# Optimization experiments

Hardware: AMD Instinct MI355X
Metric: run time of the kernel (lower is better)

The kernel has to match this reference:

```python
import jax, jax.numpy as jnp
import numpy as np

HIDDEN = 1024
NUM_HEADS = 4
HEAD_DIM = HIDDEN // NUM_HEADS
SCALE = HEAD_DIM ** -0.5
EPS = 1e-5


def setup_inputs() -> dict:
    key = jax.random.key(0)
    ks = jax.random.split(key, 8)
    B, S, D = 4, 2048, HIDDEN
    x = jax.random.normal(ks[0], (B, S, D), dtype=jnp.float32)
    attention_mask = jnp.ones((B, S), dtype=jnp.int32)
    init = 1.0 / np.sqrt(D)
    Wq = jax.random.uniform(ks[1], (D, D), jnp.float32, -init, init)
    Wk = jax.random.uniform(ks[2], (D, D), jnp.float32, -init, init)
    Wv = jax.random.uniform(ks[3], (D, D), jnp.float32, -init, init)
    Wo = jax.random.uniform(ks[4], (D, D), jnp.float32, -init, init)
    bo = jax.random.uniform(ks[5], (D,), jnp.float32, -init, init)
    gamma = jnp.ones((D,), dtype=jnp.float32)
    beta = jnp.zeros((D,), dtype=jnp.float32)
    return {"x": x, "attention_mask": attention_mask, "Wq": Wq, "Wk": Wk,
            "Wv": Wv, "Wo": Wo, "bo": bo, "gamma": gamma, "beta": beta}


def reference(x, attention_mask, Wq, Wk, Wv, Wo, bo, gamma, beta):
    # Linear layers: y = x @ W^T (torch nn.Linear convention), no bias for q/k/v
    q = jnp.einsum('bsd,ed->bse', x, Wq)
    k = jnp.einsum('bsd,ed->bse', x, Wk)
    v = jnp.einsum('bsd,ed->bse', x, Wv)
    # Full-width attention (module never splits heads), scale = head_dim^-0.5
    scores = jnp.einsum('bqd,bkd->bqk', q, k) * SCALE  # [B,S,S]
    mask = attention_mask[:, None, :]  # [B,1,S]
    scores = jnp.where(mask == 0, jnp.float32(-1e9), scores)
    attn = jax.nn.softmax(scores, axis=-1)
    ctx = jnp.einsum('bqk,bkd->bqd', attn, v)
    out = jnp.einsum('bsd,ed->bse', ctx, Wo) + bo
    # residual + LayerNorm
    h = out + x
    mu = jnp.mean(h, axis=-1, keepdims=True)
    var = jnp.mean(jnp.square(h - mu), axis=-1, keepdims=True)
    return (h - mu) * jax.lax.rsqrt(var + EPS) * gamma + beta
```

## Files before the change

### kernel.cpp

```cpp
#include <hip/hip_runtime.h>

typedef __bf16 bf16;
typedef __bf16 bf16x8 __attribute__((ext_vector_type(8)));
typedef __bf16 bf16x4 __attribute__((ext_vector_type(4)));
typedef float floatx4 __attribute__((ext_vector_type(4)));

#define HIDDEN 1024
#define SEQ 2048
#define BATCH 4
#define ATT_SCALE 0.0625f
#define LN_EPS 1e-5f

__device__ __forceinline__ void gload_lds16(const void* g, void* l) {
    __builtin_amdgcn_global_load_lds(
        (const __attribute__((address_space(1))) unsigned int*)g,
        (__attribute__((address_space(3))) unsigned int*)l, 16, 0, 0);
}

#define GBAR() asm volatile("s_barrier" ::: "memory")
#define MFMA(a, b, c) __builtin_amdgcn_mfma_f32_16x16x32_bf16(a, b, c, 0, 0, 0)

__global__ void cvt_f32_bf16(const float* __restrict__ in, bf16* __restrict__ out, int n4) {
    int i = blockIdx.x * blockDim.x + threadIdx.x;
    if (i >= n4) return;
    float4 v = ((const float4*)in)[i];
    bf16x4 o;
    o[0] = (bf16)v.x; o[1] = (bf16)v.y; o[2] = (bf16)v.z; o[3] = (bf16)v.w;
    ((bf16x4*)out)[i] = o;
}

__global__ void transpose_w3(const float* __restrict__ s0, const float* __restrict__ s1,
                             const float* __restrict__ s2,
                             bf16* __restrict__ d0p, bf16* __restrict__ d1p, bf16* __restrict__ d2p) {
    const float* in = (blockIdx.z == 0) ? s0 : (blockIdx.z == 1) ? s1 : s2;
    bf16* out = (blockIdx.z == 0) ? d0p : (blockIdx.z == 1) ? d1p : d2p;
    __shared__ __attribute__((aligned(16))) bf16 tile[64][72];
    const int d0 = blockIdx.x * 64;
    const int f0 = blockIdx.y * 64;
    const int t = threadIdx.x;
    const int r = t >> 4;
    const int c = (t & 15) * 4;
#pragma unroll
    for (int i = 0; i < 4; ++i) {
        float4 v = *(const float4*)&in[(long)(f0 + r + i * 16) * HIDDEN + d0 + c];
        bf16x4 b;
        b[0] = (bf16)v.x; b[1] = (bf16)v.y; b[2] = (bf16)v.z; b[3] = (bf16)v.w;
        *(bf16x4*)&tile[r + i * 16][c] = b;
    }
    __syncthreads();
#pragma unroll
    for (int i = 0; i < 4; ++i) {
        const int dr = r + i * 16;
        bf16x4 o;
#pragma unroll
        for (int j = 0; j < 4; ++j) o[j] = tile[c + j][dr];
        *(bf16x4*)&out[(long)(d0 + dr) * HIDDEN + f0 + c] = o;
    }
}

template <int BNv, int MODE>
__global__ __launch_bounds__(512, 2)
void gemm256(const bf16* A, const bf16* Bw, void* __restrict__ Cout,
             const float* __restrict__ bias, const float* __restrict__ resid,
             int lda, int ldb, int ldc, int K, float scale,
             long sA, long sB, long sC) {
    constexpr int ABY = 256 * 128;
    constexpr int BBY = BNv * 128;
    constexpr int SLOT = ABY + BBY;
    constexpr int AU = ABY / 8192;
    constexpr int BU = BBY / 8192;
    constexpr int WMc = (BNv == 256) ? 2 : 4;
    constexpr int WNc = (BNv == 256) ? 4 : 2;
    constexpr int MR = (BNv == 256) ? 8 : 4;
    constexpr int MH = MR / 2;

    __shared__ __attribute__((aligned(16))) char lds[2 * SLOT];

    const int gx = gridDim.x;
    const int nblk = gx * gridDim.y;
    const int bid = blockIdx.y * gx + blockIdx.x;
    const int cpx = nblk >> 3;
    const int sbid = (nblk & 7) ? bid : (bid & 7) * cpx + (bid >> 3);
    const int bx = sbid % gx, by = sbid / gx;

    const int z = blockIdx.z;
    const char* Ab = (const char*)(A + (long)z * sA);
    const char* Bb = (const char*)(Bw + (long)z * sB);
    const long lda2 = lda * 2L, ldb2 = ldb * 2L;

    const int t = threadIdx.x;
    const int lane = t & 63;
    const int w = t >> 6;
    const int wm = w / WNc, wn = w % WNc;
    const int l15 = lane & 15;
    const int l4 = lane >> 4;

    const int row0 = by * 256;
    const int col0 = bx * BNv;

    const int srow = t >> 3;
    const int soff = (((t & 7) - (srow & 7)) & 7) * 16;
    const char* aP = Ab + (long)(row0 + srow) * lda2 + soff;
    const char* bP = Bb + (long)(col0 + srow) * ldb2 + soff;
    const int ld16 = t * 16;

    auto STAGE = [&](int slot, long koff) {
        char* base = &lds[slot * SLOT];
#pragma unroll
        for (int u = 0; u < AU; ++u)
            gload_lds16(aP + u * 64 * lda2 + koff, base + u * 8192 + ld16);
#pragma unroll
        for (int u = 0; u < BU; ++u)
            gload_lds16(bP + u * 64 * ldb2 + koff, base + ABY + u * 8192 + ld16);
    };

    floatx4 acc[MR][4] = {};
    const int nk = K / 64;

    STAGE(0, 0);
    asm volatile("s_waitcnt vmcnt(0)" ::: "memory");
    GBAR();

    for (int tt = 0; tt < nk; ++tt) {
        const char* sb = &lds[(tt & 1) * SLOT];
        const int ns = (tt + 1) & 1;

        bf16x8 af[MH][2], b0[2][2], b1[2][2];

        auto RDA = [&](int m, int kkh) {
            int lr = wm * (MR * 16) + m * 16 + l15;
            return *(const bf16x8*)(sb + lr * 128 + (((kkh * 4 + l4 + lr) & 7) << 4));
        };
        auto RDB = [&](int n, int kkh) {
            int lr = wn * 64 + n * 16 + l15;
            return *(const bf16x8*)(sb + ABY + lr * 128 + (((kkh * 4 + l4 + lr) & 7) << 4));
        };

#pragma unroll
        for (int m = 0; m < MH; ++m) { af[m][0] = RDA(m, 0); af[m][1] = RDA(m, 1); }
#pragma unroll
        for (int n = 0; n < 2; ++n) { b0[n][0] = RDB(n, 0); b0[n][1] = RDB(n, 1); }
        if (tt + 1 < nk) STAGE(ns, (long)(tt + 1) * 128);
        GBAR();
        asm volatile("s_waitcnt lgkmcnt(0)" ::: "memory");
        __builtin_amdgcn_s_setprio(1);
#pragma unroll
        for (int m = 0; m < MH; ++m)
#pragma unroll
            for (int n = 0; n < 2; ++n) {
                acc[m][n] = MFMA(af[m][0], b0[n][0], acc[m][n]);
                acc[m][n] = MFMA(af[m][1], b0[n][1], acc[m][n]);
            }
        __builtin_amdgcn_s_setprio(0);
        GBAR();

#pragma unroll
        for (int n = 0; n < 2; ++n) { b1[n][0] = RDB(2 + n, 0); b1[n][1] = RDB(2 + n, 1); }
        GBAR();
        asm volatile("s_waitcnt lgkmcnt(0)" ::: "memory");
        __builtin_amdgcn_s_setprio(1);
#pragma unroll
        for (int m = 0; m < MH; ++m)
#pragma unroll
            for (int n = 0; n < 2; ++n) {
                acc[m][2 + n] = MFMA(af[m][0], b1[n][0], acc[m][2 + n]);
                acc[m][2 + n] = MFMA(af[m][1], b1[n][1], acc[m][2 + n]);
            }
        __builtin_amdgcn_s_setprio(0);

        if constexpr (BNv == 256) {
            GBAR();
#pragma unroll
            for (int m = 0; m < MH; ++m) { af[m][0] = RDA(MH + m, 0); af[m][1] = RDA(MH + m, 1); }
            GBAR();
            asm volatile("s_waitcnt lgkmcnt(0)" ::: "memory");
            __builtin_amdgcn_s_setprio(1);
#pragma unroll
            for (int m = 0; m < MH; ++m)
#pragma unroll
                for (int n = 0; n < 2; ++n) {
                    acc[MH + m][n] = MFMA(af[m][0], b0[n][0], acc[MH + m][n]);
                    acc[MH + m][n] = MFMA(af[m][1], b0[n][1], acc[MH + m][n]);
                }
            __builtin_amdgcn_s_setprio(0);
            GBAR();

            __builtin_amdgcn_s_setprio(1);
#pragma unroll
            for (int m = 0; m < MH; ++m)
#pragma unroll
                for (int n = 0; n < 2; ++n) {
                    acc[MH + m][2 + n] = MFMA(af[m][0], b1[n][0], acc[MH + m][2 + n]);
                    acc[MH + m][2 + n] = MFMA(af[m][1], b1[n][1], acc[MH + m][2 + n]);
                }
            __builtin_amdgcn_s_setprio(0);
        }

        asm volatile("s_waitcnt vmcnt(0)" ::: "memory");
        GBAR();
    }

    const int rq = l4 * 4;
    if constexpr (MODE == 0) {
        bf16* C = ((bf16*)Cout) + (long)z * sC;
#pragma unroll
        for (int m = 0; m < MR; ++m)
#pragma unroll
            for (int i = 0; i < 4; ++i) {
                long gr = row0 + wm * (MR * 16) + m * 16 + rq + i;
#pragma unroll
                for (int n = 0; n < 4; ++n) {
                    int gc = col0 + wn * 64 + n * 16 + l15;
                    C[gr * ldc + gc] = (bf16)(acc[m][n][i] * scale);
                }
            }
    } else {
        float* C = (float*)Cout + (long)z * sC;
        const float* R = resid + (long)z * sC;
#pragma unroll
        for (int m = 0; m < MR; ++m)
#pragma unroll
            for (int i = 0; i < 4; ++i) {
                long gr = row0 + wm * (MR * 16) + m * 16 + rq + i;
#pragma unroll
                for (int n = 0; n < 4; ++n) {
                    int gc = col0 + wn * 64 + n * 16 + l15;
                    C[gr * ldc + gc] = acc[m][n][i] + bias[gc] + R[gr * ldc + gc];
                }
            }
    }
}

__global__ void transpose_v(const bf16* __restrict__ yv, bf16* __restrict__ out) {
    __shared__ __attribute__((aligned(16))) bf16 tile[64][72];
    const int z = blockIdx.z;
    const bf16* ib = yv + (long)z * SEQ * 2048 + 1024;
    bf16* ob = out + (long)z * SEQ * HIDDEN;
    const int d0 = blockIdx.x * 64;
    const int s0 = blockIdx.y * 64;
    const int t = threadIdx.x;
    const int r = t >> 4;
    const int c = (t & 15) * 4;
#pragma unroll
    for (int i = 0; i < 4; ++i) {
        bf16x4 v = *(const bf16x4*)&ib[(long)(s0 + r + i * 16) * 2048 + d0 + c];
        *(bf16x4*)&tile[r + i * 16][c] = v;
    }
    __syncthreads();
#pragma unroll
    for (int i = 0; i < 4; ++i) {
        const int dr = r + i * 16;
        bf16x4 o;
#pragma unroll
        for (int j = 0; j < 4; ++j) o[j] = tile[c + j][dr];
        *(bf16x4*)&ob[(long)(d0 + dr) * SEQ + s0 + c] = o;
    }
}

__global__ void softmax_rows(bf16* __restrict__ S, const int* __restrict__ mask) {
    const int b = blockIdx.y;
    const int row = blockIdx.x;
    bf16* srow = S + ((long)b * SEQ + row) * SEQ;
    const int* mrow = mask + b * SEQ;
    const int t = threadIdx.x;

    bf16x8 sv = *(const bf16x8*)&srow[t * 8];
    int4 m0 = ((const int4*)mrow)[t * 2];
    int4 m1 = ((const int4*)mrow)[t * 2 + 1];
    int mk[8] = {m0.x, m0.y, m0.z, m0.w, m1.x, m1.y, m1.z, m1.w};

    float v[8];
    float mx = -1e30f;
#pragma unroll
    for (int j = 0; j < 8; ++j) {
        float s = (float)sv[j];
        if (mk[j] == 0) s = -1e9f;
        v[j] = s;
        mx = fmaxf(mx, s);
    }
    __shared__ float redm[4], reds[4];
#pragma unroll
    for (int off = 32; off > 0; off >>= 1) mx = fmaxf(mx, __shfl_down(mx, off));
    if ((t & 63) == 0) redm[t >> 6] = mx;
    __syncthreads();
    mx = fmaxf(fmaxf(redm[0], redm[1]), fmaxf(redm[2], redm[3]));

    float sum = 0.f;
#pragma unroll
    for (int j = 0; j < 8; ++j) {
        v[j] = __expf(v[j] - mx);
        sum += v[j];
    }
#pragma unroll
    for (int off = 32; off > 0; off >>= 1) sum += __shfl_down(sum, off);
    if ((t & 63) == 0) reds[t >> 6] = sum;
    __syncthreads();
    sum = reds[0] + reds[1] + reds[2] + reds[3];
    float inv = 1.0f / sum;

    bf16x8 o;
#pragma unroll
    for (int j = 0; j < 8; ++j) o[j] = (bf16)(v[j] * inv);
    *(bf16x8*)&srow[t * 8] = o;
}

__global__ void layernorm_out(const float* __restrict__ h, const float* __restrict__ gamma,
                              const float* __restrict__ beta, float* __restrict__ out) {
    const long row = blockIdx.x;
    const float* hr = h + row * HIDDEN;
    const int t = threadIdx.x;
    float4 v = ((const float4*)hr)[t];
    float s = v.x + v.y + v.z + v.w;
    float sq = v.x * v.x + v.y * v.y + v.z * v.z + v.w * v.w;
    __shared__ float rs[4], rq[4];
#pragma unroll
    for (int off = 32; off > 0; off >>= 1) {
        s += __shfl_down(s, off);
        sq += __shfl_down(sq, off);
    }
    if ((t & 63) == 0) { rs[t >> 6] = s; rq[t >> 6] = sq; }
    __syncthreads();
    s = rs[0] + rs[1] + rs[2] + rs[3];
    sq = rq[0] + rq[1] + rq[2] + rq[3];
    float mu = s * (1.0f / HIDDEN);
    float var = sq * (1.0f / HIDDEN) - mu * mu;
    float rinv = rsqrtf(var + LN_EPS);
    float4 g = ((const float4*)gamma)[t];
    float4 bt = ((const float4*)beta)[t];
    float4 o;
    o.x = (v.x - mu) * rinv * g.x + bt.x;
    o.y = (v.y - mu) * rinv * g.y + bt.y;
    o.z = (v.z - mu) * rinv * g.z + bt.z;
    o.w = (v.w - mu) * rinv * g.w + bt.w;
    ((float4*)(out + row * HIDDEN))[t] = o;
}

extern "C" void kernel_launch(void* const* d_in, const int* in_sizes, int n_in,
                              void* d_out, int out_size, void* d_ws, size_t ws_size,
                              hipStream_t stream) {
    const float* x     = (const float*)d_in[0];
    const int*   mask  = (const int*)d_in[1];
    const float* Wq    = (const float*)d_in[2];
    const float* Wk    = (const float*)d_in[3];
    const float* Wv    = (const float*)d_in[4];
    const float* Wo    = (const float*)d_in[5];
    const float* bo    = (const float*)d_in[6];
    const float* gamma = (const float*)d_in[7];
    const float* beta  = (const float*)d_in[8];
    float* out = (float*)d_out;

    char* ws = (char*)d_ws;
    const long MB = 1024L * 1024L;
    bf16* yv   = (bf16*)(ws + 0 * MB);
    float* h   = (float*)(ws + 0 * MB);
    bf16* xb   = (bf16*)(ws + 32 * MB);
    bf16* vt   = (bf16*)(ws + 48 * MB);
    bf16* wgc  = (bf16*)(ws + 64 * MB);
    bf16* wkT  = (bf16*)(ws + 68 * MB);
    bf16* wo   = (bf16*)(ws + 70 * MB);
    bf16* wqT  = (bf16*)(ws + 72 * MB);
    bf16* wvT  = (bf16*)(ws + 74 * MB);
    bf16* S    = (bf16*)(ws + 76 * MB);

    const int BS = BATCH * SEQ;
    const int WW = HIDDEN * HIDDEN;
    dim3 blk256(256), blk512(512);

    cvt_f32_bf16<<<dim3(BS * HIDDEN / 4 / 256), blk256, 0, stream>>>(x, xb, BS * HIDDEN / 4);
    cvt_f32_bf16<<<dim3(WW / 4 / 256), blk256, 0, stream>>>(Wo, wo, WW / 4);
    transpose_w3<<<dim3(16, 16, 3), blk256, 0, stream>>>(Wq, Wk, Wv, wqT, wkT, wvT);

    gemm256<128, 0><<<dim3(HIDDEN / 128, 2048 / 256, 2), blk512, 0, stream>>>(
        wkT, wqT, wgc, nullptr, nullptr, HIDDEN, HIDDEN, HIDDEN, HIDDEN, 1.0f,
        (long)WW, (long)WW, (long)WW);

    gemm256<256, 0><<<dim3(2048 / 256, BS / 256, 1), blk512, 0, stream>>>(
        xb, wgc, yv, nullptr, nullptr, HIDDEN, HIDDEN, 2048, HIDDEN, 1.0f, 0, 0, 0);

    transpose_v<<<dim3(HIDDEN / 64, SEQ / 64, BATCH), blk256, 0, stream>>>(yv, vt);

    gemm256<256, 0><<<dim3(SEQ / 256, SEQ / 256, BATCH), blk512, 0, stream>>>(
        yv, xb, S, nullptr, nullptr, 2048, HIDDEN, SEQ, HIDDEN, ATT_SCALE,
        (long)SEQ * 2048, (long)SEQ * HIDDEN, (long)SEQ * SEQ);

    softmax_rows<<<dim3(SEQ, BATCH), blk256, 0, stream>>>(S, mask);

    gemm256<128, 2><<<dim3(HIDDEN / 128, SEQ / 256, BATCH), blk512, 0, stream>>>(
        S, vt, h, bo, x, SEQ, SEQ, HIDDEN, SEQ, 1.0f,
        (long)SEQ * SEQ, (long)HIDDEN * SEQ, (long)SEQ * HIDDEN);

    layernorm_out<<<dim3(BS), blk256, 0, stream>>>(h, gamma, beta, out);
}
```

Measured before the change: 187.1 us.

## Drop intra-iteration barriers in GEMM main loop and shrink weight-product grid

```diff
diff --git a/kernel.cpp b/kernel.cpp
--- a/kernel.cpp
+++ b/kernel.cpp
@@ -69,7 +69,6 @@
     constexpr int SLOT = ABY + BBY;
     constexpr int AU = ABY / 8192;
     constexpr int BU = BBY / 8192;
-    constexpr int WMc = (BNv == 256) ? 2 : 4;
     constexpr int WNc = (BNv == 256) ? 4 : 2;
     constexpr int MR = (BNv == 256) ? 8 : 4;
     constexpr int MH = MR / 2;
@@ -123,9 +122,6 @@
 
     for (int tt = 0; tt < nk; ++tt) {
         const char* sb = &lds[(tt & 1) * SLOT];
-        const int ns = (tt + 1) & 1;
-
-        bf16x8 af[MH][2], b0[2][2], b1[2][2];
 
         auto RDA = [&](int m, int kkh) {
             int lr = wm * (MR * 16) + m * 16 + l15;
@@ -136,65 +132,53 @@
             return *(const bf16x8*)(sb + ABY + lr * 128 + (((kkh * 4 + l4 + lr) & 7) << 4));
         };
 
-#pragma unroll
-        for (int m = 0; m < MH; ++m) { af[m][0] = RDA(m, 0); af[m][1] = RDA(m, 1); }
-#pragma unroll
-        for (int n = 0; n < 2; ++n) { b0[n][0] = RDB(n, 0); b0[n][1] = RDB(n, 1); }
-        if (tt + 1 < nk) STAGE(ns, (long)(tt + 1) * 128);
-        GBAR();
-        asm volatile("s_waitcnt lgkmcnt(0)" ::: "memory");
+        bf16x8 alo[MH][2], ahi[MH][2], b0[2][2], b1[2][2];
+#pragma unroll
+        for (int m = 0; m < MH; ++m) { alo[m][0] = RDA(m, 0); alo[m][1] = RDA(m, 1); }
+#pragma unroll
+        for (int n = 0; n < 2; ++n) {
+            b0[n][0] = RDB(n, 0); b0[n][1] = RDB(n, 1);
+            b1[n][0] = RDB(2 + n, 0); b1[n][1] = RDB(2 + n, 1);
+        }
+
+        if (tt + 1 < nk) STAGE((tt + 1) & 1, (long)(tt + 1) * 128);
+
         __builtin_amdgcn_s_setprio(1);
 #pragma unroll
         for (int m = 0; m < MH; ++m)
 #pragma unroll
             for (int n = 0; n < 2; ++n) {
-                acc[m][n] = MFMA(af[m][0], b0[n][0], acc[m][n]);
-                acc[m][n] = MFMA(af[m][1], b0[n][1], acc[m][n]);
+                acc[m][n] = MFMA(alo[m][0], b0[n][0], acc[m][n]);
+                acc[m][n] = MFMA(alo[m][1], b0[n][1], acc[m][n]);
             }
         __builtin_amdgcn_s_setprio(0);
-        GBAR();
-
-#pragma unroll
-        for (int n = 0; n < 2; ++n) { b1[n][0] = RDB(2 + n, 0); b1[n][1] = RDB(2 + n, 1); }
-        GBAR();
-        asm volatile("s_waitcnt lgkmcnt(0)" ::: "memory");
+
+#pragma unroll
+        for (int m = 0; m < MH; ++m) { ahi[m][0] = RDA(MH + m, 0); ahi[m][1] = RDA(MH + m, 1); }
+
         __builtin_amdgcn_s_setprio(1);
 #pragma unroll
         for (int m = 0; m < MH; ++m)
 #pragma unroll
             for (int n = 0; n < 2; ++n) {
-                acc[m][2 + n] = MFMA(af[m][0], b1[n][0], acc[m][2 + n]);
-                acc[m][2 + n] = MFMA(af[m][1], b1[n][1], acc[m][2 + n]);
+                acc[m][2 + n] = MFMA(alo[m][0], b1[n][0], acc[m][2 + n]);
+                acc[m][2 + n] = MFMA(alo[m][1], b1[n][1], acc[m][2 + n]);
+            }
+#pragma unroll
+        for (int m = 0; m < MH; ++m)
+#pragma unroll
+            for (int n = 0; n < 2; ++n) {
+                acc[MH + m][n] = MFMA(ahi[m][0], b0[n][0], acc[MH + m][n]);
+                acc[MH + m][n] = MFMA(ahi[m][1], b0[n][1], acc[MH + m][n]);
+            }
+#pragma unroll
+        for (int m = 0; m < MH; ++m)
+#pragma unroll
+            for (int n = 0; n < 2; ++n) {
+                acc[MH + m][2 + n] = MFMA(ahi[m][0], b1[n][0], acc[MH + m][2 + n]);
+                acc[MH + m][2 + n] = MFMA(ahi[m][1], b1[n][1], acc[MH + m][2 + n]);
             }
         __builtin_amdgcn_s_setprio(0);
-
-        if constexpr (BNv == 256) {
-            GBAR();
-#pragma unroll
-            for (int m = 0; m < MH; ++m) { af[m][0] = RDA(MH + m, 0); af[m][1] = RDA(MH + m, 1); }
-            GBAR();
-            asm volatile("s_waitcnt lgkmcnt(0)" ::: "memory");
-            __builtin_amdgcn_s_setprio(1);
-#pragma unroll
-            for (int m = 0; m < MH; ++m)
-#pragma unroll
-                for (int n = 0; n < 2; ++n) {
-                    acc[MH + m][n] = MFMA(af[m][0], b0[n][0], acc[MH + m][n]);
-                    acc[MH + m][n] = MFMA(af[m][1], b0[n][1], acc[MH + m][n]);
-                }
-            __builtin_amdgcn_s_setprio(0);
-            GBAR();
-
-            __builtin_amdgcn_s_setprio(1);
-#pragma unroll
-            for (int m = 0; m < MH; ++m)
-#pragma unroll
-                for (int n = 0; n < 2; ++n) {
-                    acc[MH + m][2 + n] = MFMA(af[m][0], b1[n][0], acc[MH + m][2 + n]);
-                    acc[MH + m][2 + n] = MFMA(af[m][1], b1[n][1], acc[MH + m][2 + n]);
-                }
-            __builtin_amdgcn_s_setprio(0);
-        }
 
         asm volatile("s_waitcnt vmcnt(0)" ::: "memory");
         GBAR();
@@ -370,7 +354,7 @@
     cvt_f32_bf16<<<dim3(WW / 4 / 256), blk256, 0, stream>>>(Wo, wo, WW / 4);
     transpose_w3<<<dim3(16, 16, 3), blk256, 0, stream>>>(Wq, Wk, Wv, wqT, wkT, wvT);
 
-    gemm256<128, 0><<<dim3(HIDDEN / 128, 2048 / 256, 2), blk512, 0, stream>>>(
+    gemm256<128, 0><<<dim3(HIDDEN / 128, HIDDEN / 256, 2), blk512, 0, stream>>>(
         wkT, wqT, wgc, nullptr, nullptr, HIDDEN, HIDDEN, HIDDEN, HIDDEN, 1.0f,
         (long)WW, (long)WW, (long)WW);
 
```

Result: faster. 181.3 us (-3.1%).
